# Kernel optimization log

Measured on AMD Instinct MI355X. Metric: run time of the kernel, lower is better.

## Reference

```python
import jax, jax.numpy as jnp
import numpy as np

G = 4      # groups (conv groups == offset groups)
KS = 3     # kernel size
DIL = 1    # dilation
PAD = 1    # padding = dilation
EPS = 1e-5 # InstanceNorm eps


def setup_inputs() -> dict:
    key = jax.random.key(0)
    k1, k2, k3, k4, k5 = jax.random.split(key, 5)
    B, C, D, H, W = 4, 64, 8, 64, 64
    Cout = 64
    Cg = C // G
    x = jax.random.normal(k1, (B, C, D, H, W), jnp.float32)
    # small offset-conv weights so predicted offsets stay within a few pixels
    w_off = jax.random.normal(k2, (2 * KS * KS * G, Cg, KS, KS), jnp.float32) * 0.01
    b_off = jax.random.normal(k3, (2 * KS * KS * G,), jnp.float32) * 0.01
    w_dc = jax.random.normal(k4, (Cout, Cg, KS, KS), jnp.float32) * (1.0 / np.sqrt(Cg * KS * KS))
    b_dc = jax.random.normal(k5, (Cout,), jnp.float32) * 0.01
    return {"x": x, "w_off": w_off, "b_off": b_off, "w_dc": w_dc, "b_dc": b_dc}


def reference(x, w_off, b_off, w_dc, b_dc):
    B, C, D, H, W = x.shape
    N = B * D
    K = KS * KS
    Cg = C // G
    # torch .view(B*D, C, H, W) is a row-major reshape of the flat buffer
    x2 = x.reshape(N, C, H, W)

    # grouped 3x3 offset conv, same padding
    off = jax.lax.conv_general_dilated(
        x2, w_off, (1, 1), [(PAD, PAD), (PAD, PAD)],
        rhs_dilation=(DIL, DIL), feature_group_count=G,
        dimension_numbers=("NCHW", "OIHW", "NCHW"),
    ) + b_off[None, :, None, None]
    off = off.reshape(N, G, K, 2, H, W)        # (y, x) offset per group/kernel-pt
    dy, dx = off[:, :, :, 0], off[:, :, :, 1]  # [N,G,K,H,W]

    # base sampling grid per kernel point
    ki, kj = jnp.meshgrid(jnp.arange(KS), jnp.arange(KS), indexing="ij")
    ki = ki.reshape(K); kj = kj.reshape(K)
    base_y = (jnp.arange(H)[None, :] - PAD + ki[:, None] * DIL).astype(jnp.float32)  # [K,H]
    base_x = (jnp.arange(W)[None, :] - PAD + kj[:, None] * DIL).astype(jnp.float32)  # [K,W]
    py = base_y[None, None, :, :, None] + dy   # [N,G,K,H,W]
    px = base_x[None, None, :, None, :] + dx

    y0 = jnp.floor(py); x0 = jnp.floor(px)
    ly = py - y0; lx = px - x0
    y0i = y0.astype(jnp.int32); x0i = x0.astype(jnp.int32)

    xg = x2.reshape(N, G, Cg, H * W)
    gather = jax.vmap(jax.vmap(lambda xf, idx: xf[:, idx]))  # over N, G

    def corner(yi, xi, w):
        valid = (yi >= 0) & (yi < H) & (xi >= 0) & (xi < W)   # zero-pad OOB
        idx = jnp.clip(yi, 0, H - 1) * W + jnp.clip(xi, 0, W - 1)
        v = gather(xg, idx.reshape(N, G, -1)).reshape(N, G, Cg, K, H, W)
        return v * (w * valid)[:, :, None]                    # broadcast over Cg

    val = (corner(y0i,     x0i,     (1 - ly) * (1 - lx))
         + corner(y0i,     x0i + 1, (1 - ly) * lx)
         + corner(y0i + 1, x0i,     ly * (1 - lx))
         + corner(y0i + 1, x0i + 1, ly * lx))                 # [N,G,Cg,K,H,W]

    wg = w_dc.reshape(G, -1, Cg, K)                           # [G,Coutg,Cg,K]
    out = jnp.einsum("gock,ngckhw->ngohw", wg, val).reshape(N, -1, H, W)
    out = out + b_dc[None, :, None, None]

    # InstanceNorm2d (affine=False, biased var) + exact GELU
    m = out.mean((-2, -1), keepdims=True)
    v = out.var((-2, -1), keepdims=True)
    out = jax.nn.gelu((out - m) * jax.lax.rsqrt(v + EPS), approximate=False)

    Cout = out.shape[1]
    return out.reshape(B, D, Cout, H, W).transpose(0, 2, 1, 3, 4)  # [B,Cout,D,H,W]
```

## Files before the change

kernel.cpp:

```cpp
#include <hip/hip_runtime.h>
#include <hip/hip_fp16.h>
#include <math.h>

#define HW 4096
#define NN 32
#define W68 68
#define RSTR 2192

typedef __attribute__((ext_vector_type(8))) _Float16 f16x8;
typedef __attribute__((ext_vector_type(2))) _Float16 h2;
typedef __attribute__((ext_vector_type(4))) float f32x4;

__device__ inline unsigned short hbits(float a) {
    _Float16 h = (_Float16)a;
    unsigned short u;
    __builtin_memcpy(&u, &h, 2);
    return u;
}
__device__ inline unsigned hpack(float a, float b) {
    auto p = __builtin_amdgcn_cvt_pkrtz(a, b);
    unsigned u;
    __builtin_memcpy(&u, &p, 4);
    return u;
}

__device__ inline int xsw(int x, int c8) {
    return ((x << 5) | (c8 << 4)) ^ (((x >> 2) & 1) << 4);
}

__global__ __launch_bounds__(256) void wperm_build(const float* __restrict__ w_off,
                                                   const float* __restrict__ w_dc,
                                                   unsigned short* __restrict__ wperm)
{
    int idx = blockIdx.x * 256 + threadIdx.x;
    int g = idx / 7680;
    int r3 = idx - g * 7680;
    int which = r3 / 2560;
    int r = r3 - which * 2560;
    int j = r & 7;
    int rest = r >> 3;
    int nn_ = rest & 15; rest >>= 4;
    int q_ = rest & 3, kp_ = rest >> 2;
    int k = q_ * 8 + j;
    int c = k & 15, tt = kp_ * 2 + (k >> 4);
    float v = 0.f;
    if (tt < 9) {
        if (which == 0)      v = w_dc[(g * 16 + nn_) * 144 + c * 9 + tt];
        else if (which == 1) v = w_off[(g * 18 + nn_) * 144 + c * 9 + tt];
        else if (nn_ < 2)    v = w_off[(g * 18 + 16 + nn_) * 144 + c * 9 + tt];
    }
    wperm[idx] = hbits(v);
}

__global__ __launch_bounds__(512, 4) void fused_conv(const float* __restrict__ x,
                                                     const unsigned short* __restrict__ wperm,
                                                     const float* __restrict__ b_off,
                                                     const float* __restrict__ b_dc,
                                                     unsigned short* __restrict__ outpre)
{
    __shared__ __attribute__((aligned(16))) unsigned short xwin[14248];
    __shared__ __attribute__((aligned(16))) unsigned short off_lds[2 * 5120];

    int bhw = blockIdx.x;
    int bx = (bhw & 7) * 128 + (bhw >> 3);
    int n = bx >> 5, g = (bx >> 3) & 3, chunk2 = bx & 7;
    int t = threadIdx.x;
    int lane = t & 63, wv = t >> 6;
    int cc = wv >> 2, lv = wv & 3;
    int nn = lane & 15, q = lane >> 4;
    int t2 = q >> 1, chh = q & 1;
    int R0 = chunk2 * 8;

    const unsigned short* wpg = wperm + g * 7680;
    const float* xgbase = x + (size_t)(n * 64 + g * 16) * HW;
    unsigned short* offp = off_lds + cc * 5120;

    {
        int col = lane;
        #pragma unroll
        for (int rr = 0; rr < 2; rr++) {
            int r = wv + rr * 8;
            if (r < 13) {
                int h = R0 + r - 2;
                uint4 lo = {0, 0, 0, 0}, hi = {0, 0, 0, 0};
                if ((unsigned)h < 64u) {
                    const float* xp = xgbase + h * 64 + col;
                    float v[16];
                    #pragma unroll
                    for (int c = 0; c < 16; c++) v[c] = xp[(size_t)c * HW];
                    lo.x = hpack(v[0], v[1]);  lo.y = hpack(v[2], v[3]);
                    lo.z = hpack(v[4], v[5]);  lo.w = hpack(v[6], v[7]);
                    hi.x = hpack(v[8], v[9]);  hi.y = hpack(v[10], v[11]);
                    hi.z = hpack(v[12], v[13]); hi.w = hpack(v[14], v[15]);
                }
                *(uint4*)((char*)xwin + r * RSTR + xsw(col + 2, 0)) = lo;
                *(uint4*)((char*)xwin + r * RSTR + xsw(col + 2, 1)) = hi;
            }
        }
        if (t < 104) {
            int r = t >> 3, rem = t & 7;
            int xc = rem >> 1, c8 = rem & 1;
            int xx = xc < 2 ? xc : xc + 64;
            uint4 z = {0, 0, 0, 0};
            *(uint4*)((char*)xwin + r * RSTR + xsw(xx, c8)) = z;
        }
    }

    int pls[4], xbs[4]; float fx_[4];
    #pragma unroll
    for (int s = 0; s < 4; s++) {
        int pl = (lv * 4 + s) * 16 + nn;
        pls[s] = pl;
        int w = ((lv * 4 + s) & 3) * 16 + nn;
        fx_[s] = (float)(w - 1);
        xbs[s] = w + 1;
    }
    int rwbase = 4 * cc + lv + 1;
    float fybase = (float)(R0 + 4 * cc + lv - 1);

    __syncthreads();

    {
        f16x8 pb0[5], pb1[5];
        #pragma unroll
        for (int kp = 0; kp < 5; kp++) {
            int fo = ((kp * 4 + q) * 16 + nn) * 8;
            pb0[kp] = *(const f16x8*)(wpg + 2560 + fo);
            pb1[kp] = *(const f16x8*)(wpg + 5120 + fo);
        }

        f32x4 acc0[4], acc1[4];
        float bv0 = b_off[g * 18 + nn];
        float bv1 = (nn < 2) ? b_off[g * 18 + 16 + nn] : 0.f;
        #pragma unroll
        for (int s = 0; s < 4; s++)
            #pragma unroll
            for (int r = 0; r < 4; r++) { acc0[s][r] = bv0; acc1[s][r] = bv1; }

        uint4 xv[2][4];
        auto stage1 = [&](int kp) {
            int ki = t2 ? (2 * kp + 1) / 3 : (2 * kp) / 3;
            int kj = t2 ? (2 * kp + 1) % 3 : (2 * kp) % 3;
            int sl = kp & 1;
            #pragma unroll
            for (int s = 0; s < 4; s++) {
                int adr = (rwbase + ki) * RSTR + xsw(xbs[s] + kj, chh);
                xv[sl][s] = *(const uint4*)((const char*)xwin + adr);
            }
        };
        stage1(0);
        #pragma unroll
        for (int kp = 0; kp < 5; kp++) {
            if (kp < 4) stage1(kp + 1);
            __builtin_amdgcn_sched_barrier(0);
            int sl = kp & 1;
            #pragma unroll
            for (int s = 0; s < 4; s++) {
                f16x8 af = *(f16x8*)&xv[sl][s];
                acc0[s] = __builtin_amdgcn_mfma_f32_16x16x32_f16(af, pb0[kp], acc0[s], 0, 0, 0);
                acc1[s] = __builtin_amdgcn_mfma_f32_16x16x32_f16(af, pb1[kp], acc1[s], 0, 0, 0);
            }
        }

        #pragma unroll
        for (int s = 0; s < 4; s++) {
            int pl = (lv * 4 + s) * 16 + q * 4;
            #pragma unroll
            for (int r = 0; r < 4; r++) {
                offp[(pl + r) * 20 + nn] = hbits(acc0[s][r]);
                if (nn < 2)
                    offp[(pl + r) * 20 + 16 + nn] = hbits(acc1[s][r]);
            }
        }
        off_lds[t * 20 + 18] = 0;
        off_lds[t * 20 + 19] = 0;
    }

    f16x8 bwr[5];
    #pragma unroll
    for (int kp = 0; kp < 5; kp++)
        bwr[kp] = *(const f16x8*)(wpg + ((kp * 4 + q) * 16 + nn) * 8);

    __syncthreads();

    f32x4 acc[4];
    float bvd = b_dc[g * 16 + nn];
    #pragma unroll
    for (int s = 0; s < 4; s++)
        #pragma unroll
        for (int r = 0; r < 4; r++) acc[s][r] = bvd;

    uint4 RA[2], RB[2], RC[2], RD[2];
    h2 rwh[2][4];
    int rinw[2], rgy[2], rgx[2];

    auto gather_x = [&](int R, int C) -> uint4 {
        uint4 out = {0, 0, 0, 0};
        int h = R - 2, w = C - 2;
        if ((unsigned)h < 64u && (unsigned)w < 64u) {
            const float* xp = xgbase + (size_t)(chh * 8) * HW + h * 64 + w;
            unsigned* o = (unsigned*)&out;
            #pragma unroll
            for (int k = 0; k < 4; k++)
                o[k] = hpack(xp[(size_t)(2 * k) * HW], xp[(size_t)(2 * k + 1) * HW]);
        }
        return out;
    };

    auto stage = [&](int u) {
        int kp = u >> 2, s = u & 3, sl = u & 1;
        int ki = t2 ? (2 * kp + 1) / 3 : (2 * kp) / 3;
        int kj = t2 ? (2 * kp + 1) % 3 : (2 * kp) % 3;
        unsigned uo = *(const unsigned*)&offp[pls[s] * 20 + 4 * kp + 2 * t2];
        h2 oo;
        __builtin_memcpy(&oo, &uo, 4);
        float py = fybase + (float)ki + (float)oo[0];
        float px = fx_[s] + (float)kj + (float)oo[1];
        float y0f = fminf(fmaxf(floorf(py), -2.f), 64.f);
        float x0f = fminf(fmaxf(floorf(px), -2.f), 64.f);
        float ly = py - y0f, lx = px - x0f;
        float my = 1.f - ly, mx = 1.f - lx;
        rwh[sl][0] = h2{(_Float16)(my * mx), (_Float16)(my * mx)};
        rwh[sl][1] = h2{(_Float16)(my * lx), (_Float16)(my * lx)};
        rwh[sl][2] = h2{(_Float16)(ly * mx), (_Float16)(ly * mx)};
        rwh[sl][3] = h2{(_Float16)(ly * lx), (_Float16)(ly * lx)};
        int y0 = (int)y0f, x0 = (int)x0f;
        int lr = y0 + 2 - R0;
        int inw = ((unsigned)lr <= 11u);
        int lrc = inw ? lr : 0;
        int xx = x0 + 2;
        int a0 = lrc * RSTR + xsw(xx, chh);
        int a1 = lrc * RSTR + xsw(xx + 1, chh);
        RA[sl] = *(const uint4*)((const char*)xwin + a0);
        RB[sl] = *(const uint4*)((const char*)xwin + a1);
        RC[sl] = *(const uint4*)((const char*)xwin + a0 + RSTR);
        RD[sl] = *(const uint4*)((const char*)xwin + a1 + RSTR);
        rinw[sl] = inw;
        rgy[sl] = y0 + 2;
        rgx[sl] = xx;
    };
    auto consume = [&](int u) {
        int kp = u >> 2, s = u & 3, sl = u & 1;
        if (!__all(rinw[sl])) {
            if (!rinw[sl]) {
                int R = rgy[sl], C = rgx[sl];
                RA[sl] = gather_x(R, C);
                RB[sl] = gather_x(R, C + 1);
                RC[sl] = gather_x(R + 1, C);
                RD[sl] = gather_x(R + 1, C + 1);
            }
        }
        const h2* A2 = (const h2*)&RA[sl];
        const h2* B2 = (const h2*)&RB[sl];
        const h2* C2 = (const h2*)&RC[sl];
        const h2* D2 = (const h2*)&RD[sl];
        h2 w0 = rwh[sl][0], w1 = rwh[sl][1], w2 = rwh[sl][2], w3 = rwh[sl][3];
        uint4 afu;
        unsigned* au = (unsigned*)&afu;
        #pragma unroll
        for (int j = 0; j < 4; j++) {
            h2 v = w0 * A2[j] + w1 * B2[j] + w2 * C2[j] + w3 * D2[j];
            __builtin_memcpy(&au[j], &v, 4);
        }
        f16x8 af = *(f16x8*)&afu;
        acc[s] = __builtin_amdgcn_mfma_f32_16x16x32_f16(af, bwr[kp], acc[s], 0, 0, 0);
    };

    stage(0);
    #pragma unroll
    for (int u = 0; u < 20; u++) {
        if (u < 19) stage(u + 1);
        __builtin_amdgcn_sched_barrier(0);
        consume(u);
    }

    __syncthreads();
    #pragma unroll
    for (int s = 0; s < 4; s++) {
        int colb = (lv * 4 + s) * 16 + q * 4;
        uint2 pk;
        pk.x = hpack(acc[s][0], acc[s][1]);
        pk.y = hpack(acc[s][2], acc[s][3]);
        *(uint2*)(off_lds + cc * 4224 + nn * 264 + colb) = pk;
    }
    __syncthreads();
    {
        int tl = t & 255;
        unsigned short* opb = outpre + (size_t)(n * 64 + g * 16) * HW
                            + (chunk2 * 2 + cc) * 256;
        #pragma unroll
        for (int p = 0; p < 2; p++) {
            int idx = p * 256 + tl;
            int ch = idx >> 5, slot = idx & 31;
            uint4 vv = *(const uint4*)(off_lds + cc * 4224 + ch * 264 + slot * 8);
            *(uint4*)(opb + (size_t)ch * HW + slot * 8) = vv;
        }
    }
}

__global__ __launch_bounds__(256) void norm_gelu(const unsigned short* __restrict__ outpre,
                                                 float* __restrict__ out)
{
    __shared__ float red[8];
    int bhw = blockIdx.x;
    int bx = (bhw & 7) * 256 + (bhw >> 3);
    int n  = bx >> 6;
    int co = bx & 63;
    int t  = threadIdx.x;

    const uint2* base = (const uint2*)(outpre + (size_t)(n * 64 + co) * HW);
    float4 v[4];
    float s = 0.f, sq = 0.f;
    #pragma unroll
    for (int r = 0; r < 4; r++) {
        uint2 u2 = base[t + r * 256];
        h2 p0, p1;
        __builtin_memcpy(&p0, &u2.x, 4);
        __builtin_memcpy(&p1, &u2.y, 4);
        v[r].x = (float)p0[0]; v[r].y = (float)p0[1];
        v[r].z = (float)p1[0]; v[r].w = (float)p1[1];
        s  += v[r].x + v[r].y + v[r].z + v[r].w;
        sq  = fmaf(v[r].x, v[r].x, sq);
        sq  = fmaf(v[r].y, v[r].y, sq);
        sq  = fmaf(v[r].z, v[r].z, sq);
        sq  = fmaf(v[r].w, v[r].w, sq);
    }
    #pragma unroll
    for (int o2 = 32; o2 > 0; o2 >>= 1) {
        s  += __shfl_down(s,  o2, 64);
        sq += __shfl_down(sq, o2, 64);
    }
    int wid = t >> 6, lane = t & 63;
    if (lane == 0) { red[wid] = s; red[4 + wid] = sq; }
    __syncthreads();
    float S  = red[0] + red[1] + red[2] + red[3];
    float SQ = red[4] + red[5] + red[6] + red[7];
    float mean = S * (1.f / 4096.f);
    float var  = SQ * (1.f / 4096.f) - mean * mean;
    float rstd = rsqrtf(var + 1e-5f);

    int b = n >> 3, d = n & 7;
    float4* outp = (float4*)(out + ((size_t)(b * 64 + co) * 8 + d) * HW);
    #pragma unroll
    for (int r = 0; r < 4; r++) {
        float xs[4] = {v[r].x, v[r].y, v[r].z, v[r].w};
        float4 res;
        float* rp = (float*)&res;
        #pragma unroll
        for (int qq = 0; qq < 4; qq++) {
            float xn = (xs[qq] - mean) * rstd;
            float u = xn * (1.5957691f + 0.0713548162f * xn * xn);
            float e = __expf(-u);
            rp[qq] = xn * __frcp_rn(1.f + e);
        }
        outp[t + r * 256] = res;
    }
}

extern "C" void kernel_launch(void* const* d_in, const int* in_sizes, int n_in,
                              void* d_out, int out_size, void* d_ws, size_t ws_size,
                              hipStream_t stream) {
    const float* x     = (const float*)d_in[0];
    const float* w_off = (const float*)d_in[1];
    const float* w_dc  = (const float*)d_in[3];
    float* out = (float*)d_out;

    unsigned short* wperm = (unsigned short*)d_ws;
    unsigned short* outpre = (unsigned short*)((char*)d_ws + 61440);

    wperm_build<<<120, 256, 0, stream>>>(w_off, w_dc, wperm);
    fused_conv <<<1024, 512, 0, stream>>>(x, wperm,
                                          (const float*)d_in[2],
                                          (const float*)d_in[4], outpre);
    norm_gelu  <<<2048, 256, 0, stream>>>(outpre, out);
}
```

Before: 122.8 us.

## Halve fused_conv row tile to 4 rows and double grid to 2048 blocks

Each fused_conv block now covers 4 output rows instead of 8. It stages a smaller 8-row halo window and a compacted offset buffer in LDS, and every wave handles 2 pixel strips instead of 4. This cuts LDS and register use per block and doubles the grid, aiming for more occupancy and better load balance. The cost is more redundant halo loading relative to useful work, since the 4 halo rows are now shared by only 4 output rows. Sampling points that fall outside the narrower window will also take the slow global-gather fallback more often.

```diff
diff --git a/kernel.cpp b/kernel.cpp
--- a/kernel.cpp
+++ b/kernel.cpp
@@ -58,46 +58,39 @@
                                                      const float* __restrict__ b_dc,
                                                      unsigned short* __restrict__ outpre)
 {
-    __shared__ __attribute__((aligned(16))) unsigned short xwin[14248];
-    __shared__ __attribute__((aligned(16))) unsigned short off_lds[2 * 5120];
+    __shared__ __attribute__((aligned(16))) unsigned short xwin[8768];
+    __shared__ __attribute__((aligned(16))) unsigned short off_lds[4608];
 
     int bhw = blockIdx.x;
-    int bx = (bhw & 7) * 128 + (bhw >> 3);
-    int n = bx >> 5, g = (bx >> 3) & 3, chunk2 = bx & 7;
+    int bx = (bhw & 7) * 256 + (bhw >> 3);
+    int n = bx >> 6, g = (bx >> 4) & 3, chunk = bx & 15;
     int t = threadIdx.x;
-    int lane = t & 63, wv = t >> 6;
-    int cc = wv >> 2, lv = wv & 3;
+    int lane = t & 63, lv = t >> 6;
     int nn = lane & 15, q = lane >> 4;
     int t2 = q >> 1, chh = q & 1;
-    int R0 = chunk2 * 8;
+    int R0 = chunk * 4;
 
     const unsigned short* wpg = wperm + g * 7680;
     const float* xgbase = x + (size_t)(n * 64 + g * 16) * HW;
-    unsigned short* offp = off_lds + cc * 5120;
 
     {
         int col = lane;
-        #pragma unroll
-        for (int rr = 0; rr < 2; rr++) {
-            int r = wv + rr * 8;
-            if (r < 13) {
-                int h = R0 + r - 2;
-                uint4 lo = {0, 0, 0, 0}, hi = {0, 0, 0, 0};
-                if ((unsigned)h < 64u) {
-                    const float* xp = xgbase + h * 64 + col;
-                    float v[16];
-                    #pragma unroll
-                    for (int c = 0; c < 16; c++) v[c] = xp[(size_t)c * HW];
-                    lo.x = hpack(v[0], v[1]);  lo.y = hpack(v[2], v[3]);
-                    lo.z = hpack(v[4], v[5]);  lo.w = hpack(v[6], v[7]);
-                    hi.x = hpack(v[8], v[9]);  hi.y = hpack(v[10], v[11]);
-                    hi.z = hpack(v[12], v[13]); hi.w = hpack(v[14], v[15]);
-                }
-                *(uint4*)((char*)xwin + r * RSTR + xsw(col + 2, 0)) = lo;
-                *(uint4*)((char*)xwin + r * RSTR + xsw(col + 2, 1)) = hi;
-            }
-        }
-        if (t < 104) {
+        int h = R0 + lv - 2;
+        uint4 lo = {0, 0, 0, 0}, hi = {0, 0, 0, 0};
+        if ((unsigned)h < 64u) {
+            const float* xp = xgbase + h * 64 + col;
+            float v[16];
+            #pragma unroll
+            for (int c = 0; c < 16; c++) v[c] = xp[(size_t)c * HW];
+            lo.x = hpack(v[0], v[1]);  lo.y = hpack(v[2], v[3]);
+            lo.z = hpack(v[4], v[5]);  lo.w = hpack(v[6], v[7]);
+            hi.x = hpack(v[8], v[9]);  hi.y = hpack(v[10], v[11]);
+            hi.z = hpack(v[12], v[13]); hi.w = hpack(v[14], v[15]);
+        }
+        *(uint4*)((char*)xwin + lv * RSTR + xsw(col + 2, 0)) = lo;
+        *(uint4*)((char*)xwin + lv * RSTR + xsw(col + 2, 1)) = hi;
+
+        if (t < 64) {
             int r = t >> 3, rem = t & 7;
             int xc = rem >> 1, c8 = rem & 1;
             int xx = xc < 2 ? xc : xc + 64;
@@ -106,17 +99,17 @@
         }
     }
 
-    int pls[4], xbs[4]; float fx_[4];
-    #pragma unroll
-    for (int s = 0; s < 4; s++) {
-        int pl = (lv * 4 + s) * 16 + nn;
-        pls[s] = pl;
-        int w = ((lv * 4 + s) & 3) * 16 + nn;
+    int pls[2], xbs[2]; float fx_[2];
+    #pragma unroll
+    for (int s = 0; s < 2; s++) {
+        int rw = 2 * lv + s;
+        pls[s] = rw * 16 + nn;
+        int w = (rw & 3) * 16 + nn;
         fx_[s] = (float)(w - 1);
         xbs[s] = w + 1;
     }
-    int rwbase = 4 * cc + lv + 1;
-    float fybase = (float)(R0 + 4 * cc + lv - 1);
+    int wr1 = (lv >> 1) + 1;
+    float fybase = (float)(R0 + (lv >> 1) - 1);
 
     __syncthreads();
 
@@ -129,22 +122,22 @@
             pb1[kp] = *(const f16x8*)(wpg + 5120 + fo);
         }
 
-        f32x4 acc0[4], acc1[4];
+        f32x4 acc0[2], acc1[2];
         float bv0 = b_off[g * 18 + nn];
         float bv1 = (nn < 2) ? b_off[g * 18 + 16 + nn] : 0.f;
         #pragma unroll
-        for (int s = 0; s < 4; s++)
+        for (int s = 0; s < 2; s++)
             #pragma unroll
             for (int r = 0; r < 4; r++) { acc0[s][r] = bv0; acc1[s][r] = bv1; }
 
-        uint4 xv[2][4];
+        uint4 xv[2][2];
         auto stage1 = [&](int kp) {
             int ki = t2 ? (2 * kp + 1) / 3 : (2 * kp) / 3;
             int kj = t2 ? (2 * kp + 1) % 3 : (2 * kp) % 3;
             int sl = kp & 1;
             #pragma unroll
-            for (int s = 0; s < 4; s++) {
-                int adr = (rwbase + ki) * RSTR + xsw(xbs[s] + kj, chh);
+            for (int s = 0; s < 2; s++) {
+                int adr = (wr1 + ki) * RSTR + xsw(xbs[s] + kj, chh);
                 xv[sl][s] = *(const uint4*)((const char*)xwin + adr);
             }
         };
@@ -155,7 +148,7 @@
             __builtin_amdgcn_sched_barrier(0);
             int sl = kp & 1;
             #pragma unroll
-            for (int s = 0; s < 4; s++) {
+            for (int s = 0; s < 2; s++) {
                 f16x8 af = *(f16x8*)&xv[sl][s];
                 acc0[s] = __builtin_amdgcn_mfma_f32_16x16x32_f16(af, pb0[kp], acc0[s], 0, 0, 0);
                 acc1[s] = __builtin_amdgcn_mfma_f32_16x16x32_f16(af, pb1[kp], acc1[s], 0, 0, 0);
@@ -163,17 +156,15 @@
         }
 
         #pragma unroll
-        for (int s = 0; s < 4; s++) {
-            int pl = (lv * 4 + s) * 16 + q * 4;
+        for (int s = 0; s < 2; s++) {
+            int pl = (2 * lv + s) * 16 + q * 4;
             #pragma unroll
             for (int r = 0; r < 4; r++) {
-                offp[(pl + r) * 20 + nn] = hbits(acc0[s][r]);
+                off_lds[(pl + r) * 18 + nn] = hbits(acc0[s][r]);
                 if (nn < 2)
-                    offp[(pl + r) * 20 + 16 + nn] = hbits(acc1[s][r]);
+                    off_lds[(pl + r) * 18 + 16 + nn] = hbits(acc1[s][r]);
             }
         }
-        off_lds[t * 20 + 18] = 0;
-        off_lds[t * 20 + 19] = 0;
     }
 
     f16x8 bwr[5];
@@ -183,10 +174,10 @@
 
     __syncthreads();
 
-    f32x4 acc[4];
+    f32x4 acc[2];
     float bvd = b_dc[g * 16 + nn];
     #pragma unroll
-    for (int s = 0; s < 4; s++)
+    for (int s = 0; s < 2; s++)
         #pragma unroll
         for (int r = 0; r < 4; r++) acc[s][r] = bvd;
 
@@ -208,10 +199,15 @@
     };
 
     auto stage = [&](int u) {
-        int kp = u >> 2, s = u & 3, sl = u & 1;
-        int ki = t2 ? (2 * kp + 1) / 3 : (2 * kp) / 3;
-        int kj = t2 ? (2 * kp + 1) % 3 : (2 * kp) % 3;
-        unsigned uo = *(const unsigned*)&offp[pls[s] * 20 + 4 * kp + 2 * t2];
+        int kp = u >> 1, s = u & 1, sl = u & 1;
+        int ki, kj, toff;
+        if (kp == 4) { ki = 2; kj = 2; toff = 16; }
+        else {
+            ki = t2 ? (2 * kp + 1) / 3 : (2 * kp) / 3;
+            kj = t2 ? (2 * kp + 1) % 3 : (2 * kp) % 3;
+            toff = 4 * kp + 2 * t2;
+        }
+        unsigned uo = *(const unsigned*)&off_lds[pls[s] * 18 + toff];
         h2 oo;
         __builtin_memcpy(&oo, &uo, 4);
         float py = fybase + (float)ki + (float)oo[0];
@@ -226,7 +222,7 @@
         rwh[sl][3] = h2{(_Float16)(ly * lx), (_Float16)(ly * lx)};
         int y0 = (int)y0f, x0 = (int)x0f;
         int lr = y0 + 2 - R0;
-        int inw = ((unsigned)lr <= 11u);
+        int inw = ((unsigned)lr <= 6u);
         int lrc = inw ? lr : 0;
         int xx = x0 + 2;
         int a0 = lrc * RSTR + xsw(xx, chh);
@@ -240,7 +236,7 @@
         rgx[sl] = xx;
     };
     auto consume = [&](int u) {
-        int kp = u >> 2, s = u & 3, sl = u & 1;
+        int kp = u >> 1, s = u & 1, sl = u & 1;
         if (!__all(rinw[sl])) {
             if (!rinw[sl]) {
                 int R = rgy[sl], C = rgx[sl];
@@ -268,33 +264,27 @@
 
     stage(0);
     #pragma unroll
-    for (int u = 0; u < 20; u++) {
-        if (u < 19) stage(u + 1);
+    for (int u = 0; u < 10; u++) {
+        if (u < 9) stage(u + 1);
         __builtin_amdgcn_sched_barrier(0);
         consume(u);
     }
 
     __syncthreads();
     #pragma unroll
-    for (int s = 0; s < 4; s++) {
-        int colb = (lv * 4 + s) * 16 + q * 4;
+    for (int s = 0; s < 2; s++) {
+        int colb = (2 * lv + s) * 16 + q * 4;
         uint2 pk;
         pk.x = hpack(acc[s][0], acc[s][1]);
         pk.y = hpack(acc[s][2], acc[s][3]);
-        *(uint2*)(off_lds + cc * 4224 + nn * 264 + colb) = pk;
+        *(uint2*)(off_lds + nn * 264 + colb) = pk;
     }
     __syncthreads();
     {
-        int tl = t & 255;
-        unsigned short* opb = outpre + (size_t)(n * 64 + g * 16) * HW
-                            + (chunk2 * 2 + cc) * 256;
-        #pragma unroll
-        for (int p = 0; p < 2; p++) {
-            int idx = p * 256 + tl;
-            int ch = idx >> 5, slot = idx & 31;
-            uint4 vv = *(const uint4*)(off_lds + cc * 4224 + ch * 264 + slot * 8);
-            *(uint4*)(opb + (size_t)ch * HW + slot * 8) = vv;
-        }
+        int ch = t >> 5, slot = t & 31;
+        unsigned short* opb = outpre + (size_t)(n * 64 + g * 16) * HW + chunk * 256;
+        uint4 vv = *(const uint4*)(off_lds + ch * 264 + slot * 8);
+        *(uint4*)(opb + (size_t)ch * HW + slot * 8) = vv;
     }
 }
 
@@ -369,7 +359,7 @@
     unsigned short* outpre = (unsigned short*)((char*)d_ws + 61440);
 
     wperm_build<<<120, 256, 0, stream>>>(w_off, w_dc, wperm);
-    fused_conv <<<1024, 512, 0, stream>>>(x, wperm,
+    fused_conv <<<2048, 512, 0, stream>>>(x, wperm,
                                           (const float*)d_in[2],
                                           (const float*)d_in[4], outpre);
     norm_gelu  <<<2048, 256, 0, stream>>>(outpre, out);
```

New measurement: 122.3 us. About the same (-0.4%).
